# Kernel optimization log

Hardware: AMD Instinct MI355X
Metric: run time of the kernel (lower is better)

Reference implementation:

```python
import jax, jax.numpy as jnp
import numpy as np

B, T, E, H = 2, 2048, 1024, 16
M1, M2 = 1024, 256
DH = E // H


def setup_inputs() -> dict:
    key = jax.random.key(0)
    ks = jax.random.split(key, 8)
    return {
        "x": jax.random.normal(ks[0], (B, T, E), dtype=jnp.float32),
        "K1": jax.random.normal(ks[1], (B, M1, E), dtype=jnp.float32),
        "V1": jax.random.normal(ks[2], (B, M1, E), dtype=jnp.float32),
        "K2": jax.random.normal(ks[3], (B, M2, E), dtype=jnp.float32),
        "V2": jax.random.normal(ks[4], (B, M2, E), dtype=jnp.float32),
        "Wq": jax.random.normal(ks[5], (E, E), dtype=jnp.float32) * (1.0 / np.sqrt(E)),
        "Wproj": jax.random.normal(ks[6], (E, E), dtype=jnp.float32) * (1.0 / np.sqrt(E)),
        "gate": jnp.asarray(-2.0, dtype=jnp.float32),
    }


def reference(x, K1, V1, K2, V2, Wq, Wproj, gate):
    Bx, Tx, Ex = x.shape
    dh = Ex // H
    scale = 1.0 / np.sqrt(dh).astype(np.float32)
    # Q: [B,T,H,dh]  (torch Linear: x @ W.T)
    Q = (x @ Wq.T).reshape(Bx, Tx, H, dh)

    def attend(Kf, Vf):
        M = Kf.shape[1]
        Kh = Kf.reshape(Bx, M, H, dh)
        Vh = Vf.reshape(Bx, M, H, dh)
        s = jnp.einsum("bthd,bmhd->bhtm", Q, Kh) * scale
        p = jax.nn.softmax(s, axis=-1)
        return jnp.einsum("bhtm,bmhd->bthd", p, Vh)

    ctx = attend(K1, V1) + attend(K2, V2)            # [B,T,H,dh]
    ctx = ctx.reshape(Bx, Tx, Ex) @ Wproj.T          # output projection
    alpha = jax.nn.sigmoid(gate)
    return alpha * ctx
```

## Files before the change

kernel.cpp:

```cpp
#include <hip/hip_runtime.h>

#define BB  2
#define TT  2048
#define EE  1024
#define HH  16
#define DH  64
#define MM1 1024
#define MM2 256

#define KSCL 0.18033688011112042f

typedef unsigned short u16;
typedef unsigned int   u32;
typedef __bf16 bf16x2 __attribute__((ext_vector_type(2)));
typedef __bf16 bf16x8 __attribute__((ext_vector_type(8)));
typedef float  f32x4  __attribute__((ext_vector_type(4)));

static __device__ __forceinline__ u32 f2bf_bits(float x) {
    union { float f; u32 u; } v; v.f = x;
    return (v.u + 0x7FFFu + ((v.u >> 16) & 1u)) >> 16;
}
static __device__ __forceinline__ u32 pkbf(float a, float b) {
    bf16x2 t; t.x = (__bf16)a; t.y = (__bf16)b;
    return __builtin_bit_cast(u32, t);
}
static __device__ __forceinline__ float fexp2(float x) {
    float r; asm("v_exp_f32 %0, %1" : "=v"(r) : "v"(x)); return r;
}
static __device__ __forceinline__ int swz(int row, int cb) {
    return row * 128 + (cb ^ ((row & 7) << 4));
}
static __device__ __forceinline__ void gload16(void* lds, const void* g) {
    __builtin_amdgcn_global_load_lds((const __attribute__((address_space(1))) u32*)g,
                                     (__attribute__((address_space(3))) u32*)lds, 16, 0, 0);
}

__global__ __launch_bounds__(256) void conv_all(const float* __restrict__ x,
                                                const float* __restrict__ wq,
                                                const float* __restrict__ wp,
                                                const float* __restrict__ K1, const float* __restrict__ V1,
                                                const float* __restrict__ K2, const float* __restrict__ V2,
                                                char* __restrict__ xs, char* __restrict__ wqs, char* __restrict__ wps,
                                                char* __restrict__ Kb1, char* __restrict__ Vb1,
                                                char* __restrict__ Kb2, char* __restrict__ Vb2)
{
    __shared__ u16 T[64 * 72];
    const int z = blockIdx.z, bx = blockIdx.x, by = blockIdx.y;
    const int tid = threadIdx.x;
    if (z < 3) {
        if (by >= 16) return;
        if (z > 0 && bx >= 8) return;
        const float* A = z == 0 ? x : (z == 1 ? wq : wp);
        char* Ab = z == 0 ? xs : (z == 1 ? wqs : wps);
        const int row = tid >> 1, half = tid & 1;
        const float* src = A + ((size_t)bx * 128 + row) * EE + by * 64 + half * 32;
        char* dst = Ab + ((size_t)(bx * 16 + by)) * 16384;
        float v[32];
        #pragma unroll
        for (int i = 0; i < 8; ++i) *(float4*)&v[i * 4] = ((const float4*)src)[i];
        u32 pk[16];
        #pragma unroll
        for (int j = 0; j < 16; ++j) pk[j] = pkbf(v[2 * j], v[2 * j + 1]);
        #pragma unroll
        for (int j = 0; j < 4; ++j)
            *(uint4*)(dst + swz(row, half * 64 + j * 16)) = *(uint4*)&pk[j * 4];
        return;
    }
    const int zz = z - 3;
    const int M = (zz >= 2) ? MM2 : MM1;
    if (bx * 64 >= M) return;
    const int isV = zz & 1;
    const float* src4[4] = { K1, V1, K2, V2 };
    char* dst4[4] = { Kb1, Vb1, Kb2, Vb2 };
    const int b = by >> 4, h = by & 15;
    char* dst = dst4[zz] + ((size_t)by * (M / 64) + bx) * 8192;
    const float* src = src4[zz] + ((size_t)b * M + (size_t)bx * 64) * EE + h * DH;
    const int m = tid >> 2, q = tid & 3;
    const float* s = src + (size_t)m * EE + q * 16;
    float v[16];
    #pragma unroll
    for (int i = 0; i < 4; ++i) *(float4*)&v[i * 4] = ((const float4*)s)[i];
    if (!isV) {
        u32 pk[8];
        #pragma unroll
        for (int j = 0; j < 8; ++j) pk[j] = pkbf(v[2 * j] * KSCL, v[2 * j + 1] * KSCL);
        *(uint4*)(dst + swz(m, q * 32))      = *(uint4*)&pk[0];
        *(uint4*)(dst + swz(m, q * 32 + 16)) = *(uint4*)&pk[4];
    } else {
        #pragma unroll
        for (int j = 0; j < 16; ++j) T[(q * 16 + j) * 72 + m] = (u16)f2bf_bits(v[j]);
        __syncthreads();
        const int d = tid >> 2, qq = tid & 3;
        uint4 a0 = *(const uint4*)((const char*)T + d * 144 + qq * 32);
        uint4 a1 = *(const uint4*)((const char*)T + d * 144 + qq * 32 + 16);
        *(uint4*)(dst + swz(d, qq * 32))      = a0;
        *(uint4*)(dst + swz(d, qq * 32 + 16)) = a1;
    }
}

template<bool FINAL>
__global__ __launch_bounds__(512) void gemm_swz(const char* __restrict__ Ab,
                                                const char* __restrict__ Bb,
                                                void* __restrict__ Cout,
                                                const float* __restrict__ gate)
{
    constexpr int NKT = EE / 64;
    __shared__ char As[2][16384];
    __shared__ char Bs[2][8192];
    const int tid = threadIdx.x, lane = tid & 63, w = tid >> 6;
    const int wr = w >> 1, wc = w & 1, g = lane >> 4, ln = lane & 15;
    int lin = blockIdx.y * 32 + blockIdx.x;
    lin = (lin & 7) * 64 + (lin >> 3);
    const int bmi = lin & 31, bni = lin >> 5;
    const char* Abase = Ab + (size_t)bmi * NKT * 16384;
    const char* Bbase = Bb + (size_t)(bni >> 1) * NKT * 16384 + (size_t)(bni & 1) * 8192;
    gload16(As[0] + tid * 16,        Abase + tid * 16);
    gload16(As[0] + tid * 16 + 8192, Abase + tid * 16 + 8192);
    gload16(Bs[0] + tid * 16,        Bbase + tid * 16);
    f32x4 acc[2][2] = {};
    for (int kt = 0; kt < NKT; ++kt) {
        const int cur = kt & 1;
        __syncthreads();
        if (kt + 1 < NKT) {
            const char* an = Abase + (size_t)(kt + 1) * 16384;
            const char* bn = Bbase + (size_t)(kt + 1) * 16384;
            gload16(As[cur ^ 1] + tid * 16,        an + tid * 16);
            gload16(As[cur ^ 1] + tid * 16 + 8192, an + tid * 16 + 8192);
            gload16(Bs[cur ^ 1] + tid * 16,        bn + tid * 16);
        }
        #pragma unroll
        for (int kh = 0; kh < 2; ++kh) {
            bf16x8 af[2], bf2[2];
            #pragma unroll
            for (int i = 0; i < 2; ++i)
                af[i] = *(const bf16x8*)(As[cur] + swz(wr * 32 + i * 16 + ln, kh * 64 + g * 16));
            #pragma unroll
            for (int j = 0; j < 2; ++j)
                bf2[j] = *(const bf16x8*)(Bs[cur] + swz(wc * 32 + j * 16 + ln, kh * 64 + g * 16));
            #pragma unroll
            for (int i = 0; i < 2; ++i)
                #pragma unroll
                for (int j = 0; j < 2; ++j)
                    acc[i][j] = __builtin_amdgcn_mfma_f32_16x16x32_bf16(af[i], bf2[j], acc[i][j], 0, 0, 0);
        }
    }
    float alpha = 1.0f;
    if constexpr (FINAL) alpha = 1.0f / (1.0f + __expf(-gate[0]));
    #pragma unroll
    for (int i = 0; i < 2; ++i)
        #pragma unroll
        for (int r = 0; r < 4; ++r) {
            const int row = bmi * 128 + wr * 32 + i * 16 + g * 4 + r;
            #pragma unroll
            for (int j = 0; j < 2; ++j) {
                const int col = bni * 64 + wc * 32 + j * 16 + ln;
                if constexpr (FINAL) ((float*)Cout)[(size_t)row * EE + col] = acc[i][j][r] * alpha;
                else ((u16*)Cout)[(size_t)row * EE + col] = (u16)f2bf_bits(acc[i][j][r]);
            }
        }
}

__global__ __launch_bounds__(512) void attn2(const u16* __restrict__ Qb,
                                             const char* __restrict__ Kb1, const char* __restrict__ Vb1,
                                             const char* __restrict__ Kb2, const char* __restrict__ Vb2,
                                             char* __restrict__ Ctxs)
{
    __shared__ char KV[2][16384];
    __shared__ char Ps[8][2048];
    const int tid = threadIdx.x, lane = tid & 63, w = tid >> 6;
    const int g = lane >> 4, ln = lane & 15;
    const int lnx = (ln & 7) << 4;
    int lin = blockIdx.y * 16 + blockIdx.x;
    lin = (lin & 7) * 64 + (lin >> 3);
    const int bx = lin & 15, bh = lin >> 4;
    const int b = bh >> 4, h = bh & 15;
    const int t0 = bx * 128;
    constexpr int NT1 = MM1 / 64, NT = NT1 + MM2 / 64;

    bf16x8 qf[2];
    #pragma unroll
    for (int kh = 0; kh < 2; ++kh)
        qf[kh] = *(const bf16x8*)(Qb + ((size_t)(b * TT + t0 + w * 16 + ln)) * EE
                                  + h * DH + kh * 32 + g * 8);

    const char* Kbase[2] = { Kb1 + (size_t)bh * (MM1 / 64) * 8192, Kb2 + (size_t)bh * (MM2 / 64) * 8192 };
    const char* Vbase[2] = { Vb1 + (size_t)bh * (MM1 / 64) * 8192, Vb2 + (size_t)bh * (MM2 / 64) * 8192 };

    gload16(KV[0] + tid * 16,        Kbase[0] + tid * 16);
    gload16(KV[0] + 8192 + tid * 16, Vbase[0] + tid * 16);

    f32x4 oacc[4] = {}, outacc[4] = {};
    float psum = 0.0f;

    for (int ti = 0; ti < NT; ++ti) {
        const int cur = ti & 1;
        __syncthreads();
        if (ti + 1 < NT) {
            const int nx = ti + 1;
            const int pn = (nx >= NT1) ? 1 : 0, mtn = pn ? nx - NT1 : nx;
            gload16(KV[cur ^ 1] + tid * 16,        Kbase[pn] + (size_t)mtn * 8192 + tid * 16);
            gload16(KV[cur ^ 1] + 8192 + tid * 16, Vbase[pn] + (size_t)mtn * 8192 + tid * 16);
        }
        f32x4 s[4] = {};
        __builtin_amdgcn_s_setprio(1);
        #pragma unroll
        for (int kh = 0; kh < 2; ++kh)
            #pragma unroll
            for (int f = 0; f < 4; ++f) {
                const bf16x8 kf = *(const bf16x8*)(KV[cur] + swz(f * 16 + ln, kh * 64 + g * 16));
                s[f] = __builtin_amdgcn_mfma_f32_16x16x32_bf16(kf, qf[kh], s[f], 0, 0, 0);
            }
        __builtin_amdgcn_s_setprio(0);
        #pragma unroll
        for (int f = 0; f < 4; ++f) {
            const float p0 = fexp2(s[f][0]);
            const float p1 = fexp2(s[f][1]);
            const float p2 = fexp2(s[f][2]);
            const float p3 = fexp2(s[f][3]);
            psum += (p0 + p1) + (p2 + p3);
            uint2 w2; w2.x = pkbf(p0, p1); w2.y = pkbf(p2, p3);
            *(uint2*)(Ps[w] + ln * 128 + ((f * 32 + g * 8) ^ lnx)) = w2;
        }
        __builtin_amdgcn_s_setprio(1);
        #pragma unroll
        for (int ks = 0; ks < 2; ++ks) {
            const bf16x8 pf = *(const bf16x8*)(Ps[w] + ln * 128 + ((ks * 64 + g * 16) ^ lnx));
            #pragma unroll
            for (int f = 0; f < 4; ++f) {
                const bf16x8 vf = *(const bf16x8*)(KV[cur] + 8192 + swz(f * 16 + ln, ks * 64 + g * 16));
                oacc[f] = __builtin_amdgcn_mfma_f32_16x16x32_bf16(vf, pf, oacc[f], 0, 0, 0);
            }
        }
        __builtin_amdgcn_s_setprio(0);
        if (ti == NT1 - 1 || ti == NT - 1) {
            float t = psum;
            t += __shfl_xor(t, 16);
            t += __shfl_xor(t, 32);
            const float inv = 1.0f / t;
            #pragma unroll
            for (int f = 0; f < 4; ++f)
                #pragma unroll
                for (int r = 0; r < 4; ++r) {
                    outacc[f][r] += oacc[f][r] * inv;
                    oacc[f][r] = 0.0f;
                }
            psum = 0.0f;
        }
    }

    __syncthreads();
    char* eb = &KV[0][0];
    #pragma unroll
    for (int f = 0; f < 4; ++f) {
        uint2 w2;
        w2.x = pkbf(outacc[f][0], outacc[f][1]);
        w2.y = pkbf(outacc[f][2], outacc[f][3]);
        *(uint2*)(eb + (w * 16 + ln) * 128 + ((f * 32 + g * 8) ^ lnx)) = w2;
    }
    __syncthreads();
    char* blob = Ctxs + ((size_t)((b * 16 + bx) * 16 + h)) * 16384;
    #pragma unroll
    for (int i = 0; i < 2; ++i)
        *(uint4*)(blob + tid * 16 + i * 8192) = *(const uint4*)(eb + tid * 16 + i * 8192);
}

extern "C" void kernel_launch(void* const* d_in, const int* in_sizes, int n_in,
                              void* d_out, int out_size, void* d_ws, size_t ws_size,
                              hipStream_t stream) {
    const float* x    = (const float*)d_in[0];
    const float* K1   = (const float*)d_in[1];
    const float* V1   = (const float*)d_in[2];
    const float* K2   = (const float*)d_in[3];
    const float* V2   = (const float*)d_in[4];
    const float* Wq   = (const float*)d_in[5];
    const float* Wp   = (const float*)d_in[6];
    const float* gate = (const float*)d_in[7];
    float* out = (float*)d_out;

    char* ws  = (char*)d_ws;
    char* Xs  = ws;
    char* Wqs = ws + (8u  << 20);
    char* Wps = ws + (10u << 20);
    u16*  Qb  = (u16*)(ws + (12u << 20));
    char* Kb1 = ws + (20u << 20);
    char* Vb1 = ws + (24u << 20);
    char* Kb2 = ws + (28u << 20);
    char* Vb2 = ws + (29u << 20);

    dim3 blk(256);
    conv_all<<<dim3(32, 32, 7), blk, 0, stream>>>(x, Wq, Wp, K1, V1, K2, V2,
                                                  Xs, Wqs, Wps, Kb1, Vb1, Kb2, Vb2);
    gemm_swz<false><<<dim3(32, 16), dim3(512), 0, stream>>>(Xs, Wqs, Qb, nullptr);
    attn2<<<dim3(16, 32), dim3(512), 0, stream>>>(Qb, Kb1, Vb1, Kb2, Vb2, Xs );
    gemm_swz<true><<<dim3(32, 16), dim3(512), 0, stream>>>(Xs, Wps, out, gate);
}
```

Before: 90.09 us.

## Triple-buffer LDS tiles with explicit vmcnt waits in GEMM and attention

Both the GEMM and attention kernels move from double to triple buffering of their shared-memory tiles. Loads are issued two iterations ahead, and each step waits with a partial s_waitcnt vmcnt plus a raw barrier instead of a full __syncthreads. The goal is to hide more global-load latency behind MFMA work. It costs more LDS per block, which may reduce occupancy, and it depends on the waitcnt counts matching the number of async loads in flight.

After: 86.63 us, median of 2. 3.8% less time.

```diff
diff --git a/kernel.cpp b/kernel.cpp
--- a/kernel.cpp
+++ b/kernel.cpp
@@ -105,8 +105,8 @@
                                                 const float* __restrict__ gate)
 {
     constexpr int NKT = EE / 64;
-    __shared__ char As[2][16384];
-    __shared__ char Bs[2][8192];
+    __shared__ char As[3][16384];
+    __shared__ char Bs[3][8192];
     const int tid = threadIdx.x, lane = tid & 63, w = tid >> 6;
     const int wr = w >> 1, wc = w & 1, g = lane >> 4, ln = lane & 15;
     int lin = blockIdx.y * 32 + blockIdx.x;
@@ -114,36 +114,47 @@
     const int bmi = lin & 31, bni = lin >> 5;
     const char* Abase = Ab + (size_t)bmi * NKT * 16384;
     const char* Bbase = Bb + (size_t)(bni >> 1) * NKT * 16384 + (size_t)(bni & 1) * 8192;
-    gload16(As[0] + tid * 16,        Abase + tid * 16);
-    gload16(As[0] + tid * 16 + 8192, Abase + tid * 16 + 8192);
-    gload16(Bs[0] + tid * 16,        Bbase + tid * 16);
     f32x4 acc[2][2] = {};
-    for (int kt = 0; kt < NKT; ++kt) {
-        const int cur = kt & 1;
-        __syncthreads();
-        if (kt + 1 < NKT) {
-            const char* an = Abase + (size_t)(kt + 1) * 16384;
-            const char* bn = Bbase + (size_t)(kt + 1) * 16384;
-            gload16(As[cur ^ 1] + tid * 16,        an + tid * 16);
-            gload16(As[cur ^ 1] + tid * 16 + 8192, an + tid * 16 + 8192);
-            gload16(Bs[cur ^ 1] + tid * 16,        bn + tid * 16);
-        }
+
+    auto stage = [&](int t, int buf) {
+        const char* an = Abase + (size_t)t * 16384;
+        const char* bn = Bbase + (size_t)t * 16384;
+        gload16(As[buf] + tid * 16,        an + tid * 16);
+        gload16(As[buf] + tid * 16 + 8192, an + tid * 16 + 8192);
+        gload16(Bs[buf] + tid * 16,        bn + tid * 16);
+    };
+    auto compute = [&](int buf) {
         #pragma unroll
         for (int kh = 0; kh < 2; ++kh) {
             bf16x8 af[2], bf2[2];
             #pragma unroll
             for (int i = 0; i < 2; ++i)
-                af[i] = *(const bf16x8*)(As[cur] + swz(wr * 32 + i * 16 + ln, kh * 64 + g * 16));
+                af[i] = *(const bf16x8*)(As[buf] + swz(wr * 32 + i * 16 + ln, kh * 64 + g * 16));
             #pragma unroll
             for (int j = 0; j < 2; ++j)
-                bf2[j] = *(const bf16x8*)(Bs[cur] + swz(wc * 32 + j * 16 + ln, kh * 64 + g * 16));
+                bf2[j] = *(const bf16x8*)(Bs[buf] + swz(wc * 32 + j * 16 + ln, kh * 64 + g * 16));
             #pragma unroll
             for (int i = 0; i < 2; ++i)
                 #pragma unroll
                 for (int j = 0; j < 2; ++j)
                     acc[i][j] = __builtin_amdgcn_mfma_f32_16x16x32_bf16(af[i], bf2[j], acc[i][j], 0, 0, 0);
         }
-    }
+    };
+
+    stage(0, 0);
+    stage(1, 1);
+    for (int kt = 0; kt < NKT - 1; ++kt) {
+        asm volatile("s_waitcnt vmcnt(3)" ::: "memory");
+        __builtin_amdgcn_s_barrier();
+        __builtin_amdgcn_sched_barrier(0);
+        if (kt + 2 < NKT) stage(kt + 2, (kt + 2) % 3);
+        compute(kt % 3);
+    }
+    asm volatile("s_waitcnt vmcnt(0)" ::: "memory");
+    __builtin_amdgcn_s_barrier();
+    __builtin_amdgcn_sched_barrier(0);
+    compute((NKT - 1) % 3);
+
     float alpha = 1.0f;
     if constexpr (FINAL) alpha = 1.0f / (1.0f + __expf(-gate[0]));
     #pragma unroll
@@ -165,7 +176,7 @@
                                              const char* __restrict__ Kb2, const char* __restrict__ Vb2,
                                              char* __restrict__ Ctxs)
 {
-    __shared__ char KV[2][16384];
+    __shared__ char KV[3][16384];
     __shared__ char Ps[8][2048];
     const int tid = threadIdx.x, lane = tid & 63, w = tid >> 6;
     const int g = lane >> 4, ln = lane & 15;
@@ -186,28 +197,22 @@
     const char* Kbase[2] = { Kb1 + (size_t)bh * (MM1 / 64) * 8192, Kb2 + (size_t)bh * (MM2 / 64) * 8192 };
     const char* Vbase[2] = { Vb1 + (size_t)bh * (MM1 / 64) * 8192, Vb2 + (size_t)bh * (MM2 / 64) * 8192 };
 
-    gload16(KV[0] + tid * 16,        Kbase[0] + tid * 16);
-    gload16(KV[0] + 8192 + tid * 16, Vbase[0] + tid * 16);
-
     f32x4 oacc[4] = {}, outacc[4] = {};
     float psum = 0.0f;
 
-    for (int ti = 0; ti < NT; ++ti) {
-        const int cur = ti & 1;
-        __syncthreads();
-        if (ti + 1 < NT) {
-            const int nx = ti + 1;
-            const int pn = (nx >= NT1) ? 1 : 0, mtn = pn ? nx - NT1 : nx;
-            gload16(KV[cur ^ 1] + tid * 16,        Kbase[pn] + (size_t)mtn * 8192 + tid * 16);
-            gload16(KV[cur ^ 1] + 8192 + tid * 16, Vbase[pn] + (size_t)mtn * 8192 + tid * 16);
-        }
+    auto stage = [&](int t, int buf) {
+        const int p = (t >= NT1) ? 1 : 0, mt = p ? t - NT1 : t;
+        gload16(KV[buf] + tid * 16,        Kbase[p] + (size_t)mt * 8192 + tid * 16);
+        gload16(KV[buf] + 8192 + tid * 16, Vbase[p] + (size_t)mt * 8192 + tid * 16);
+    };
+    auto compute = [&](int buf, int ti) {
         f32x4 s[4] = {};
         __builtin_amdgcn_s_setprio(1);
         #pragma unroll
         for (int kh = 0; kh < 2; ++kh)
             #pragma unroll
             for (int f = 0; f < 4; ++f) {
-                const bf16x8 kf = *(const bf16x8*)(KV[cur] + swz(f * 16 + ln, kh * 64 + g * 16));
+                const bf16x8 kf = *(const bf16x8*)(KV[buf] + swz(f * 16 + ln, kh * 64 + g * 16));
                 s[f] = __builtin_amdgcn_mfma_f32_16x16x32_bf16(kf, qf[kh], s[f], 0, 0, 0);
             }
         __builtin_amdgcn_s_setprio(0);
@@ -227,7 +232,7 @@
             const bf16x8 pf = *(const bf16x8*)(Ps[w] + ln * 128 + ((ks * 64 + g * 16) ^ lnx));
             #pragma unroll
             for (int f = 0; f < 4; ++f) {
-                const bf16x8 vf = *(const bf16x8*)(KV[cur] + 8192 + swz(f * 16 + ln, ks * 64 + g * 16));
+                const bf16x8 vf = *(const bf16x8*)(KV[buf] + 8192 + swz(f * 16 + ln, ks * 64 + g * 16));
                 oacc[f] = __builtin_amdgcn_mfma_f32_16x16x32_bf16(vf, pf, oacc[f], 0, 0, 0);
             }
         }
@@ -246,7 +251,21 @@
                 }
             psum = 0.0f;
         }
-    }
+    };
+
+    stage(0, 0);
+    stage(1, 1);
+    for (int ti = 0; ti < NT - 1; ++ti) {
+        asm volatile("s_waitcnt vmcnt(2)" ::: "memory");
+        __builtin_amdgcn_s_barrier();
+        __builtin_amdgcn_sched_barrier(0);
+        if (ti + 2 < NT) stage(ti + 2, (ti + 2) % 3);
+        compute(ti % 3, ti);
+    }
+    asm volatile("s_waitcnt vmcnt(0)" ::: "memory");
+    __builtin_amdgcn_s_barrier();
+    __builtin_amdgcn_sched_barrier(0);
+    compute((NT - 1) % 3, NT - 1);
 
     __syncthreads();
     char* eb = &KV[0][0];
```
